# Kernel optimization log

Measured on AMD Instinct MI355X. Metric: run time of the kernel, lower is better.

Reference implementation:

```python
import jax, jax.numpy as jnp
import numpy as np
from jax import lax

NUM_CLASSES = 80
TOPK = 1000
CONF_THRESH = 0.05
NMS_THRESH = 0.6
MAX_COORD = 4096.0  # > any box coordinate; used for class-aware NMS offset trick
N_ANCHORS = 262144


def setup_inputs() -> dict:
    key = jax.random.key(0)
    k1, k2, k3 = jax.random.split(key, 3)
    # classification logits; shift down so sigmoid scores are mostly below conf_thresh
    cls_pred = jax.random.normal(k1, (1, N_ANCHORS, NUM_CLASSES), jnp.float32) * 2.0 - 2.0
    # valid xyxy boxes in absolute pixel coords (image ~1024)
    xy = jax.random.uniform(k2, (1, N_ANCHORS, 2), jnp.float32) * 1000.0
    wh = jax.random.uniform(k3, (1, N_ANCHORS, 2), jnp.float32) * 200.0 + 4.0
    box_pred = jnp.concatenate([xy, xy + wh], axis=-1)
    return {"cls_pred": cls_pred, "box_pred": box_pred, "img_h": 1024, "img_w": 1024}


def _pairwise_iou(b):
    # b: [K, 4] xyxy -> [K, K] IoU
    x1, y1, x2, y2 = b[:, 0], b[:, 1], b[:, 2], b[:, 3]
    area = (x2 - x1) * (y2 - y1)
    ix1 = jnp.maximum(x1[:, None], x1[None, :])
    iy1 = jnp.maximum(y1[:, None], y1[None, :])
    ix2 = jnp.minimum(x2[:, None], x2[None, :])
    iy2 = jnp.minimum(y2[:, None], y2[None, :])
    inter = jnp.clip(ix2 - ix1, 0.0) * jnp.clip(iy2 - iy1, 0.0)
    return inter / (area[:, None] + area[None, :] - inter + 1e-9)


def reference(cls_pred, box_pred, img_h, img_w):
    cls_p = cls_pred[0]          # [N, C]
    box_p = box_pred[0]          # [N, 4]
    # sigmoid + flatten + descending sort + slice(topk)  ==  top_k on flat scores
    scores_all = jax.nn.sigmoid(cls_p).reshape(-1)            # [N*C]
    top_scores, top_idxs = lax.top_k(scores_all, TOPK)        # sorted descending
    valid = top_scores > CONF_THRESH                          # keep mask (fixed size)
    labels = top_idxs % NUM_CLASSES
    anchor_idxs = top_idxs // NUM_CLASSES
    boxes = box_p[anchor_idxs]                                # [K, 4]

    # class-aware (per-class) greedy NMS via coordinate offset trick
    offset = labels.astype(boxes.dtype)[:, None] * MAX_COORD
    iou = _pairwise_iou(boxes + offset)                       # [K, K]
    idx = jnp.arange(TOPK)

    def body(i, keep):
        sup = keep[i] & (iou[i] > NMS_THRESH) & (idx > i)
        return keep & ~sup

    keep = lax.fori_loop(0, TOPK, body, valid)

    # normalize boxes to [0, 1] by image size and clip (as inference_single_image)
    scale = jnp.array([img_w, img_h, img_w, img_h], dtype=boxes.dtype)
    boxes_norm = jnp.clip(boxes / scale, 0.0, 1.0)

    scores_out = jnp.where(keep, top_scores, 0.0)
    return boxes_norm, scores_out, labels, keep
```

## Files before the change

### kernel.cpp

```cpp
#include <hip/hip_runtime.h>
#include <stdint.h>

#define NUM_CLASSES 80u
#define TOPK 1000
#define CONF_T 0.05f
#define NMS_T 0.6f
#define MAX_COORD 4096.0f
#define TARGET 1152u
#define CAP 49152u
#define SRVCAP 2048u
#define STATIC_F 4.0f
#define STATIC_KEY 0xC0800000u
#define NBINS 4096
#define BINSH 13
#define LCAP 512u
#define PBLK 1024u

typedef unsigned long long ull;
typedef ull ull2 __attribute__((ext_vector_type(2)));

__device__ __forceinline__ uint32_t fkey(float x) {
  uint32_t k = __float_as_uint(x);
  return (k & 0x80000000u) ? ~k : (k | 0x80000000u);
}

__device__ __forceinline__ uint32_t suffix_scan_256(uint32_t v, uint32_t* part,
                                                    int t) {
  int lane = t & 63, wid = t >> 6;
#pragma unroll
  for (int off = 1; off < 64; off <<= 1) {
    uint32_t x = __shfl_down(v, off);
    if (lane + off < 64) v += x;
  }
  if (lane == 0) part[wid] = v;
  __syncthreads();
  if (wid == 0 && lane < 4) {
    uint32_t pv = part[lane];
#pragma unroll
    for (int off = 1; off < 4; off <<= 1) {
      uint32_t x = __shfl_down(pv, off);
      if (lane + off < 4) pv += x;
    }
    part[lane] = pv;
  }
  __syncthreads();
  uint32_t after = (wid < 3) ? part[wid + 1] : 0u;
  return v + after;
}

template <int NBINSX>
__device__ __forceinline__ void pick_bin(const uint32_t* hl, uint32_t target,
                                         int t, uint32_t* part, uint32_t* binS,
                                         uint32_t* AS, uint32_t* cntS) {
  const int CH = NBINSX / 256;
  uint32_t s = 0;
#pragma unroll
  for (int j = 0; j < CH; ++j) s += hl[t * CH + j];
  uint32_t incl = suffix_scan_256(s, part, t);
  uint32_t after = incl - s;
  if (incl >= target && after < target) {
    uint32_t cum = after;
    for (int j = CH - 1; j >= 0; --j) {
      uint32_t h = hl[t * CH + j];
      if (cum + h >= target) { *binS = (uint32_t)(t * CH + j); *AS = cum; *cntS = h; break; }
      cum += h;
    }
  }
}

__global__ void __launch_bounds__(256) kz(uint32_t* sel, float* out,
                                          float* topScore) {
  int g = blockIdx.x * 256 + threadIdx.x;
  if (g < 16) sel[g] = 0u;
  for (int i = g; i < 4000; i += 4096) out[i] = 0.0f;
  if (g < 1000) { out[5000 + g] = 0.0f; topScore[g] = 0.0f; }
}

__global__ void __launch_bounds__(256) kA(const float4* __restrict__ cls, int n4,
                                          uint32_t* __restrict__ sel,
                                          uint32_t* __restrict__ candKey,
                                          uint32_t* __restrict__ candIdx) {
  __shared__ uint32_t lk[LCAP];
  __shared__ uint32_t li[LCAP];
  __shared__ uint32_t lcnt, gbase;
  if (threadIdx.x == 0) lcnt = 0u;
  __syncthreads();
  int stride = gridDim.x * blockDim.x;
  for (int i = blockIdx.x * blockDim.x + threadIdx.x; i < n4; i += stride) {
    float4 v = cls[i];
    float f4[4] = {v.x, v.y, v.z, v.w};
#pragma unroll
    for (int c = 0; c < 4; ++c) {
      if (f4[c] >= STATIC_F) {
        uint32_t p = atomicAdd(&lcnt, 1u);
        if (p < LCAP) { lk[p] = fkey(f4[c]); li[p] = (uint32_t)i * 4u + c; }
        else {
          uint32_t gp = atomicAdd(&sel[2], 1u);
          if (gp < CAP) { candKey[gp] = fkey(f4[c]); candIdx[gp] = (uint32_t)i * 4u + c; }
        }
      }
    }
  }
  __syncthreads();
  uint32_t c = lcnt; if (c > LCAP) c = LCAP;
  if (threadIdx.x == 0 && c) gbase = atomicAdd(&sel[2], c);
  __syncthreads();
  for (uint32_t i = threadIdx.x; i < c; i += 256u) {
    uint32_t gp = gbase + i;
    if (gp < CAP) { candKey[gp] = lk[i]; candIdx[gp] = li[i]; }
  }
}

__global__ void __launch_bounds__(256) kSel(
    const float4* __restrict__ cls4, int n4,
    uint32_t* __restrict__ sel,
    const uint32_t* __restrict__ candKey, const uint32_t* __restrict__ candIdx,
    ull* __restrict__ srv) {
  __shared__ uint32_t hl[NBINS];
  __shared__ uint32_t part[16];
  __shared__ uint32_t sk_[PBLK];
  __shared__ uint32_t si_[PBLK];
  __shared__ uint32_t lcnt, gbase, binS, AS, cntS;
  int t = threadIdx.x;
  uint32_t n = sel[2];
  bool fb = (n < TARGET) || (n > CAP);

  if (!fb) {
    for (int i = t; i < NBINS; i += 256) hl[i] = 0u;
    if (t == 0) { lcnt = 0u; binS = 0u; AS = 0u; cntS = 0u; }
    __syncthreads();
    const uint4* ck4 = (const uint4*)candKey;
    uint32_t n4c = n >> 2;
    for (uint32_t i = t; i < n4c; i += 256u) {
      uint4 kv = ck4[i];
      uint32_t b0 = (kv.x - STATIC_KEY) >> BINSH; if (b0 > NBINS - 1u) b0 = NBINS - 1u;
      uint32_t b1 = (kv.y - STATIC_KEY) >> BINSH; if (b1 > NBINS - 1u) b1 = NBINS - 1u;
      uint32_t b2 = (kv.z - STATIC_KEY) >> BINSH; if (b2 > NBINS - 1u) b2 = NBINS - 1u;
      uint32_t b3 = (kv.w - STATIC_KEY) >> BINSH; if (b3 > NBINS - 1u) b3 = NBINS - 1u;
      atomicAdd(&hl[b0], 1u); atomicAdd(&hl[b1], 1u);
      atomicAdd(&hl[b2], 1u); atomicAdd(&hl[b3], 1u);
    }
    for (uint32_t i = (n4c << 2) + (uint32_t)t; i < n; i += 256u) {
      uint32_t b = (candKey[i] - STATIC_KEY) >> BINSH;
      if (b > NBINS - 1u) b = NBINS - 1u;
      atomicAdd(&hl[b], 1u);
    }
    __syncthreads();
    pick_bin<NBINS>(hl, TARGET, t, part, &binS, &AS, &cntS);
    __syncthreads();
    uint32_t T;
    if (AS + cntS > SRVCAP)
      T = STATIC_KEY + ((binS + 1u) << BINSH);
    else
      T = STATIC_KEY + (binS << BINSH);
    uint32_t stride = gridDim.x * blockDim.x;
    for (uint32_t i = blockIdx.x * 256u + (uint32_t)t; i < n; i += stride) {
      uint32_t k = candKey[i];
      if (k >= T) {
        uint32_t p = atomicAdd(&lcnt, 1u);
        if (p < PBLK) { sk_[p] = k; si_[p] = candIdx[i]; }
      }
    }
    __syncthreads();
    uint32_t c = lcnt; if (c > PBLK) c = PBLK;
    if (t == 0 && c) gbase = atomicAdd(&sel[4], c);
    __syncthreads();
    for (uint32_t i = t; i < c; i += 256u) {
      uint32_t k = sk_[i];
      float x = __uint_as_float(k & 0x7fffffffu);
      float p = 1.0f / (1.0f + expf(-x));
      uint32_t pos = gbase + i;
      if (pos < SRVCAP)
        srv[pos] = ((ull)__float_as_uint(p) << 32) | (ull)(uint32_t)(~si_[i]);
    }
  } else {
    if (blockIdx.x != 0) return;
    for (int i = t; i < NBINS; i += 256) hl[i] = 0u;
    if (t == 0) { binS = 0u; AS = 0u; cntS = 0u; }
    __syncthreads();
    for (int i = t; i < n4; i += 256) {
      float4 v = cls4[i];
      atomicAdd(&hl[fkey(v.x) >> 20], 1u);
      atomicAdd(&hl[fkey(v.y) >> 20], 1u);
      atomicAdd(&hl[fkey(v.z) >> 20], 1u);
      atomicAdd(&hl[fkey(v.w) >> 20], 1u);
    }
    __syncthreads();
    pick_bin<NBINS>(hl, TARGET, t, part, &binS, &AS, &cntS);
    __syncthreads();
    uint32_t b20 = binS, A = AS;
    for (int i = t; i < 1024; i += 256) hl[i] = 0u;
    if (t == 0) { binS = 0u; }
    __syncthreads();
    for (int i = t; i < n4; i += 256) {
      float4 v = cls4[i];
      uint32_t k4[4] = {fkey(v.x), fkey(v.y), fkey(v.z), fkey(v.w)};
#pragma unroll
      for (int c2 = 0; c2 < 4; ++c2)
        if ((k4[c2] >> 20) == b20) atomicAdd(&hl[(k4[c2] >> 10) & 1023u], 1u);
    }
    __syncthreads();
    uint32_t rem = TARGET - A;
    pick_bin<1024>(hl, rem, t, part, &binS, &AS, &cntS);
    __syncthreads();
    uint32_t T = (b20 << 20) | (binS << 10);
    for (int i = t; i < n4; i += 256) {
      float4 v = cls4[i];
      uint32_t k4[4] = {fkey(v.x), fkey(v.y), fkey(v.z), fkey(v.w)};
#pragma unroll
      for (int c2 = 0; c2 < 4; ++c2) {
        uint32_t k = k4[c2];
        if (k >= T) {
          uint32_t pos = atomicAdd(&sel[4], 1u);
          if (pos < SRVCAP) {
            float x = (k & 0x80000000u) ? __uint_as_float(k & 0x7fffffffu)
                                        : __uint_as_float(~k);
            float p = 1.0f / (1.0f + expf(-x));
            uint32_t idx = (uint32_t)i * 4u + c2;
            srv[pos] = ((ull)__float_as_uint(p) << 32) | (ull)(uint32_t)(~idx);
          }
        }
      }
    }
  }
}

__global__ void __launch_bounds__(256) kF2(
    const float* __restrict__ box, const int* __restrict__ ph,
    const int* __restrict__ pw, const uint32_t* __restrict__ sel,
    const ull* __restrict__ srv, float* __restrict__ out,
    float* __restrict__ topScore, float* __restrict__ obox) {
  __shared__ __align__(16) ull sk[SRVCAP];
  int t = threadIdx.x;
  uint32_t scount = sel[4]; if (scount > SRVCAP) scount = SRVCAP;
  uint32_t pad = (scount + 1u) & ~1u;
  for (uint32_t i = t; i < pad; i += 256u) sk[i] = (i < scount) ? srv[i] : 0ull;
  __syncthreads();
  uint32_t i = blockIdx.x * 256u + (uint32_t)t;
  if (i >= scount) return;
  ull my = sk[i];
  uint32_t rank = 0;
#pragma unroll 4
  for (uint32_t j = 0; j < pad; j += 2u) {
    ull2 v = *reinterpret_cast<const ull2*>(&sk[j]);
    rank += (v.x > my) + (v.y > my);
  }
  if (rank >= TOPK) return;
  uint32_t idx = ~(uint32_t)my;
  float p = __uint_as_float((uint32_t)(my >> 32));
  uint32_t label = idx % NUM_CLASSES;
  uint32_t anchor = idx / NUM_CLASSES;
  float W = (float)pw[0], H = (float)ph[0];
  float b0 = box[anchor * 4u + 0u], b1 = box[anchor * 4u + 1u];
  float b2 = box[anchor * 4u + 2u], b3 = box[anchor * 4u + 3u];
  out[rank * 4 + 0] = fminf(fmaxf(b0 / W, 0.0f), 1.0f);
  out[rank * 4 + 1] = fminf(fmaxf(b1 / H, 0.0f), 1.0f);
  out[rank * 4 + 2] = fminf(fmaxf(b2 / W, 0.0f), 1.0f);
  out[rank * 4 + 3] = fminf(fmaxf(b3 / H, 0.0f), 1.0f);
  out[5000 + rank] = (float)label;
  topScore[rank] = p;
  float off = (float)label * MAX_COORD;
  obox[rank * 4 + 0] = b0 + off; obox[rank * 4 + 1] = b1 + off;
  obox[rank * 4 + 2] = b2 + off; obox[rank * 4 + 3] = b3 + off;
}

__global__ void kG(const float* __restrict__ obox, ull* __restrict__ masks,
                   uint32_t* __restrict__ rowsum) {
  __shared__ uint32_t rsS;
  int i = blockIdx.x;
  if (threadIdx.x == 0) rsS = 0u;
  __syncthreads();
  float x1i = obox[i * 4 + 0], y1i = obox[i * 4 + 1];
  float x2i = obox[i * 4 + 2], y2i = obox[i * 4 + 3];
  float ai = (x2i - x1i) * (y2i - y1i);
  for (int base = 0; base < 1024; base += 256) {
    int jj = base + (int)threadIdx.x;
    bool bit = false;
    if (jj < TOPK && jj > i) {
      float x1j = obox[jj * 4 + 0], y1j = obox[jj * 4 + 1];
      float x2j = obox[jj * 4 + 2], y2j = obox[jj * 4 + 3];
      float aj = (x2j - x1j) * (y2j - y1j);
      float ix1 = fmaxf(x1i, x1j), iy1 = fmaxf(y1i, y1j);
      float ix2 = fminf(x2i, x2j), iy2 = fminf(y2i, y2j);
      float iw = fmaxf(ix2 - ix1, 0.0f), ih = fmaxf(iy2 - iy1, 0.0f);
      float inter = iw * ih;
      float iou = inter / (ai + aj - inter + 1e-9f);
      bit = iou > NMS_T;
    }
    ull m = __ballot(bit);
    if ((threadIdx.x & 63u) == 0u) {
      masks[i * 16 + (jj >> 6)] = m;
      if (m) atomicOr(&rsS, 1u << (jj >> 6));
    }
  }
  __syncthreads();
  if (threadIdx.x == 0) rowsum[i] = rsS;
}

__global__ void __launch_bounds__(256) kH(const float* __restrict__ topScore,
                                          const ull* __restrict__ masks,
                                          const uint32_t* __restrict__ rowsum,
                                          float* __restrict__ out) {
  __shared__ ull lmask[TOPK * 16];
  __shared__ uint32_t rsL[TOPK];
  __shared__ ull keepsh[16];
  int t = threadIdx.x;
  for (int i = t; i < TOPK; i += 256) rsL[i] = rowsum[i];
  if (t < 16) keepsh[t] = 0ull;
  __syncthreads();
  for (int i = t; i < TOPK * 16; i += 256) {
    lmask[i] = ((rsL[i >> 4] >> (i & 15)) & 1u) ? masks[i] : 0ull;
  }
  for (int base = 0; base < 1024; base += 256) {
    int r = base + t;
    bool v = (r < TOPK) && (topScore[r] > CONF_T);
    ull b = __ballot(v);
    if ((t & 63) == 0) keepsh[(base >> 6) + (t >> 6)] = b;
  }
  __syncthreads();
  if (t < 64) {
    ull kw = (t < 16) ? keepsh[t] : 0ull;
    ull nzw = 0ull;
    if (t < 16) {
      for (int b = 0; b < 64; ++b) {
        int r = t * 64 + b;
        if (r < TOPK && rsL[r]) nzw |= 1ull << b;
      }
    }
    for (int w = 0; w < 16; ++w) {
      ull cur = __shfl(kw, w) & __shfl(nzw, w);
      while (cur) {
        int b = __ffsll((long long)cur) - 1;
        int i = w * 64 + b;
        if (t < 16) kw &= ~lmask[i * 16 + t];
        ull nk = __shfl(kw, w);
        cur = nk & __shfl(nzw, w);
        cur &= (b == 63) ? 0ull : (~0ull << (b + 1));
      }
    }
    if (t < 16) keepsh[t] = kw;
  }
  __syncthreads();
  for (int r = t; r < TOPK; r += 256) {
    bool k = (keepsh[r >> 6] >> (r & 63)) & 1ull;
    float s = topScore[r];
    out[4000 + r] = k ? s : 0.0f;
    out[6000 + r] = k ? 1.0f : 0.0f;
  }
}

extern "C" void kernel_launch(void* const* d_in, const int* in_sizes, int n_in,
                              void* d_out, int out_size, void* d_ws, size_t ws_size,
                              hipStream_t stream) {
  const float* cls = (const float*)d_in[0];
  const float* box = (const float*)d_in[1];
  const int* ph = (const int*)d_in[2];
  const int* pw = (const int*)d_in[3];
  float* out = (float*)d_out;
  int n = in_sizes[0];

  uint8_t* w = (uint8_t*)d_ws;
  uint32_t* sel     = (uint32_t*)(w + 16384);
  uint32_t* candKey = (uint32_t*)(w + 20480);
  uint32_t* candIdx = (uint32_t*)(w + 20480 + (size_t)CAP * 4);
  ull*      srv     = (ull*)     (w + 20480 + (size_t)CAP * 8);
  float*    topScore= (float*)   (w + 20480 + (size_t)CAP * 8 + 16384);
  float*    obox    = (float*)   (w + 20480 + (size_t)CAP * 8 + 16384 + 4096);
  ull*      masks   = (ull*)     (w + 20480 + (size_t)CAP * 8 + 16384 + 4096 + 16384);
  uint32_t* rowsum  = (uint32_t*)(w + 20480 + (size_t)CAP * 8 + 16384 + 4096 + 16384 + 131072);

  kz  <<<16, 256, 0, stream>>>(sel, out, topScore);
  kA  <<<2048, 256, 0, stream>>>((const float4*)cls, n / 4, sel, candKey, candIdx);
  kSel<<<64, 256, 0, stream>>>((const float4*)cls, n / 4, sel, candKey, candIdx, srv);
  kF2 <<<SRVCAP / 256, 256, 0, stream>>>(box, ph, pw, sel, srv, out, topScore, obox);
  kG  <<<TOPK, 256, 0, stream>>>(obox, masks, rowsum);
  kH  <<<1, 256, 0, stream>>>(topScore, masks, rowsum, out);
}
```

Measured before the change: 192.5 us.

## Fuse threshold selection and rank-scatter into one kernel using shared memory

Merges the selection kernel and the rank/scatter kernel into a single kSF kernel. Each of 16 blocks redundantly rebuilds the histogram and collects the full survivor set into shared memory, then ranks only the survivors assigned to it by index modulo 16. Sigmoid is deferred to the final emit step. This removes one launch and the global srv round-trip, at the cost of redundant histogram and compaction work per block and fewer blocks for the O(n^2) rank step.

```diff
diff --git a/kernel.cpp b/kernel.cpp
--- a/kernel.cpp
+++ b/kernel.cpp
@@ -14,7 +14,7 @@
 #define NBINS 4096
 #define BINSH 13
 #define LCAP 512u
-#define PBLK 1024u
+#define SFBLK 16u
 
 typedef unsigned long long ull;
 typedef ull ull2 __attribute__((ext_vector_type(2)));
@@ -111,146 +111,19 @@
   }
 }
 
-__global__ void __launch_bounds__(256) kSel(
-    const float4* __restrict__ cls4, int n4,
-    uint32_t* __restrict__ sel,
-    const uint32_t* __restrict__ candKey, const uint32_t* __restrict__ candIdx,
-    ull* __restrict__ srv) {
-  __shared__ uint32_t hl[NBINS];
-  __shared__ uint32_t part[16];
-  __shared__ uint32_t sk_[PBLK];
-  __shared__ uint32_t si_[PBLK];
-  __shared__ uint32_t lcnt, gbase, binS, AS, cntS;
-  int t = threadIdx.x;
-  uint32_t n = sel[2];
-  bool fb = (n < TARGET) || (n > CAP);
-
-  if (!fb) {
-    for (int i = t; i < NBINS; i += 256) hl[i] = 0u;
-    if (t == 0) { lcnt = 0u; binS = 0u; AS = 0u; cntS = 0u; }
-    __syncthreads();
-    const uint4* ck4 = (const uint4*)candKey;
-    uint32_t n4c = n >> 2;
-    for (uint32_t i = t; i < n4c; i += 256u) {
-      uint4 kv = ck4[i];
-      uint32_t b0 = (kv.x - STATIC_KEY) >> BINSH; if (b0 > NBINS - 1u) b0 = NBINS - 1u;
-      uint32_t b1 = (kv.y - STATIC_KEY) >> BINSH; if (b1 > NBINS - 1u) b1 = NBINS - 1u;
-      uint32_t b2 = (kv.z - STATIC_KEY) >> BINSH; if (b2 > NBINS - 1u) b2 = NBINS - 1u;
-      uint32_t b3 = (kv.w - STATIC_KEY) >> BINSH; if (b3 > NBINS - 1u) b3 = NBINS - 1u;
-      atomicAdd(&hl[b0], 1u); atomicAdd(&hl[b1], 1u);
-      atomicAdd(&hl[b2], 1u); atomicAdd(&hl[b3], 1u);
-    }
-    for (uint32_t i = (n4c << 2) + (uint32_t)t; i < n; i += 256u) {
-      uint32_t b = (candKey[i] - STATIC_KEY) >> BINSH;
-      if (b > NBINS - 1u) b = NBINS - 1u;
-      atomicAdd(&hl[b], 1u);
-    }
-    __syncthreads();
-    pick_bin<NBINS>(hl, TARGET, t, part, &binS, &AS, &cntS);
-    __syncthreads();
-    uint32_t T;
-    if (AS + cntS > SRVCAP)
-      T = STATIC_KEY + ((binS + 1u) << BINSH);
-    else
-      T = STATIC_KEY + (binS << BINSH);
-    uint32_t stride = gridDim.x * blockDim.x;
-    for (uint32_t i = blockIdx.x * 256u + (uint32_t)t; i < n; i += stride) {
-      uint32_t k = candKey[i];
-      if (k >= T) {
-        uint32_t p = atomicAdd(&lcnt, 1u);
-        if (p < PBLK) { sk_[p] = k; si_[p] = candIdx[i]; }
-      }
-    }
-    __syncthreads();
-    uint32_t c = lcnt; if (c > PBLK) c = PBLK;
-    if (t == 0 && c) gbase = atomicAdd(&sel[4], c);
-    __syncthreads();
-    for (uint32_t i = t; i < c; i += 256u) {
-      uint32_t k = sk_[i];
-      float x = __uint_as_float(k & 0x7fffffffu);
-      float p = 1.0f / (1.0f + expf(-x));
-      uint32_t pos = gbase + i;
-      if (pos < SRVCAP)
-        srv[pos] = ((ull)__float_as_uint(p) << 32) | (ull)(uint32_t)(~si_[i]);
-    }
-  } else {
-    if (blockIdx.x != 0) return;
-    for (int i = t; i < NBINS; i += 256) hl[i] = 0u;
-    if (t == 0) { binS = 0u; AS = 0u; cntS = 0u; }
-    __syncthreads();
-    for (int i = t; i < n4; i += 256) {
-      float4 v = cls4[i];
-      atomicAdd(&hl[fkey(v.x) >> 20], 1u);
-      atomicAdd(&hl[fkey(v.y) >> 20], 1u);
-      atomicAdd(&hl[fkey(v.z) >> 20], 1u);
-      atomicAdd(&hl[fkey(v.w) >> 20], 1u);
-    }
-    __syncthreads();
-    pick_bin<NBINS>(hl, TARGET, t, part, &binS, &AS, &cntS);
-    __syncthreads();
-    uint32_t b20 = binS, A = AS;
-    for (int i = t; i < 1024; i += 256) hl[i] = 0u;
-    if (t == 0) { binS = 0u; }
-    __syncthreads();
-    for (int i = t; i < n4; i += 256) {
-      float4 v = cls4[i];
-      uint32_t k4[4] = {fkey(v.x), fkey(v.y), fkey(v.z), fkey(v.w)};
-#pragma unroll
-      for (int c2 = 0; c2 < 4; ++c2)
-        if ((k4[c2] >> 20) == b20) atomicAdd(&hl[(k4[c2] >> 10) & 1023u], 1u);
-    }
-    __syncthreads();
-    uint32_t rem = TARGET - A;
-    pick_bin<1024>(hl, rem, t, part, &binS, &AS, &cntS);
-    __syncthreads();
-    uint32_t T = (b20 << 20) | (binS << 10);
-    for (int i = t; i < n4; i += 256) {
-      float4 v = cls4[i];
-      uint32_t k4[4] = {fkey(v.x), fkey(v.y), fkey(v.z), fkey(v.w)};
-#pragma unroll
-      for (int c2 = 0; c2 < 4; ++c2) {
-        uint32_t k = k4[c2];
-        if (k >= T) {
-          uint32_t pos = atomicAdd(&sel[4], 1u);
-          if (pos < SRVCAP) {
-            float x = (k & 0x80000000u) ? __uint_as_float(k & 0x7fffffffu)
-                                        : __uint_as_float(~k);
-            float p = 1.0f / (1.0f + expf(-x));
-            uint32_t idx = (uint32_t)i * 4u + c2;
-            srv[pos] = ((ull)__float_as_uint(p) << 32) | (ull)(uint32_t)(~idx);
-          }
-        }
-      }
-    }
-  }
-}
-
-__global__ void __launch_bounds__(256) kF2(
-    const float* __restrict__ box, const int* __restrict__ ph,
-    const int* __restrict__ pw, const uint32_t* __restrict__ sel,
-    const ull* __restrict__ srv, float* __restrict__ out,
-    float* __restrict__ topScore, float* __restrict__ obox) {
-  __shared__ __align__(16) ull sk[SRVCAP];
-  int t = threadIdx.x;
-  uint32_t scount = sel[4]; if (scount > SRVCAP) scount = SRVCAP;
-  uint32_t pad = (scount + 1u) & ~1u;
-  for (uint32_t i = t; i < pad; i += 256u) sk[i] = (i < scount) ? srv[i] : 0ull;
-  __syncthreads();
-  uint32_t i = blockIdx.x * 256u + (uint32_t)t;
-  if (i >= scount) return;
-  ull my = sk[i];
-  uint32_t rank = 0;
-#pragma unroll 4
-  for (uint32_t j = 0; j < pad; j += 2u) {
-    ull2 v = *reinterpret_cast<const ull2*>(&sk[j]);
-    rank += (v.x > my) + (v.y > my);
-  }
-  if (rank >= TOPK) return;
+__device__ __forceinline__ void emit_one(ull my, uint32_t rank,
+                                         const float* __restrict__ box,
+                                         float W, float H,
+                                         float* __restrict__ out,
+                                         float* __restrict__ topScore,
+                                         float* __restrict__ obox) {
   uint32_t idx = ~(uint32_t)my;
-  float p = __uint_as_float((uint32_t)(my >> 32));
+  uint32_t kk = (uint32_t)(my >> 32);
+  float x = (kk & 0x80000000u) ? __uint_as_float(kk & 0x7fffffffu)
+                               : __uint_as_float(~kk);
+  float p = 1.0f / (1.0f + expf(-x));
   uint32_t label = idx % NUM_CLASSES;
   uint32_t anchor = idx / NUM_CLASSES;
-  float W = (float)pw[0], H = (float)ph[0];
   float b0 = box[anchor * 4u + 0u], b1 = box[anchor * 4u + 1u];
   float b2 = box[anchor * 4u + 2u], b3 = box[anchor * 4u + 3u];
   out[rank * 4 + 0] = fminf(fmaxf(b0 / W, 0.0f), 1.0f);
@@ -262,6 +135,139 @@
   float off = (float)label * MAX_COORD;
   obox[rank * 4 + 0] = b0 + off; obox[rank * 4 + 1] = b1 + off;
   obox[rank * 4 + 2] = b2 + off; obox[rank * 4 + 3] = b3 + off;
+}
+
+__global__ void __launch_bounds__(256) kSF(
+    const float4* __restrict__ cls4, int n4,
+    const uint32_t* __restrict__ sel,
+    const uint32_t* __restrict__ candKey, const uint32_t* __restrict__ candIdx,
+    const float* __restrict__ box, const int* __restrict__ ph,
+    const int* __restrict__ pw, float* __restrict__ out,
+    float* __restrict__ topScore, float* __restrict__ obox) {
+  __shared__ uint32_t hl[NBINS];
+  __shared__ __align__(16) ull sk64[SRVCAP];
+  __shared__ uint32_t part[16];
+  __shared__ uint32_t lcnt, binS, AS, cntS;
+  int t = threadIdx.x;
+  uint32_t b = blockIdx.x;
+  uint32_t n = sel[2];
+  bool fb = (n < TARGET) || (n > CAP);
+  float W = (float)pw[0], H = (float)ph[0];
+
+  if (!fb) {
+    for (int i = t; i < NBINS; i += 256) hl[i] = 0u;
+    if (t == 0) { lcnt = 0u; binS = 0u; AS = 0u; cntS = 0u; }
+    __syncthreads();
+    const uint4* ck4 = (const uint4*)candKey;
+    uint32_t n4c = n >> 2;
+    for (uint32_t i = t; i < n4c; i += 256u) {
+      uint4 kv = ck4[i];
+      uint32_t b0 = (kv.x - STATIC_KEY) >> BINSH; if (b0 > NBINS - 1u) b0 = NBINS - 1u;
+      uint32_t b1 = (kv.y - STATIC_KEY) >> BINSH; if (b1 > NBINS - 1u) b1 = NBINS - 1u;
+      uint32_t b2 = (kv.z - STATIC_KEY) >> BINSH; if (b2 > NBINS - 1u) b2 = NBINS - 1u;
+      uint32_t b3 = (kv.w - STATIC_KEY) >> BINSH; if (b3 > NBINS - 1u) b3 = NBINS - 1u;
+      atomicAdd(&hl[b0], 1u); atomicAdd(&hl[b1], 1u);
+      atomicAdd(&hl[b2], 1u); atomicAdd(&hl[b3], 1u);
+    }
+    for (uint32_t i = (n4c << 2) + (uint32_t)t; i < n; i += 256u) {
+      uint32_t bb = (candKey[i] - STATIC_KEY) >> BINSH;
+      if (bb > NBINS - 1u) bb = NBINS - 1u;
+      atomicAdd(&hl[bb], 1u);
+    }
+    __syncthreads();
+    pick_bin<NBINS>(hl, TARGET, t, part, &binS, &AS, &cntS);
+    __syncthreads();
+    uint32_t T;
+    if (AS + cntS > SRVCAP)
+      T = STATIC_KEY + ((binS + 1u) << BINSH);
+    else
+      T = STATIC_KEY + (binS << BINSH);
+    for (uint32_t i = t; i < n; i += 256u) {
+      uint32_t k = candKey[i];
+      if (k >= T) {
+        uint32_t p = atomicAdd(&lcnt, 1u);
+        if (p < SRVCAP)
+          sk64[p] = ((ull)k << 32) | (ull)(uint32_t)(~candIdx[i]);
+      }
+    }
+    __syncthreads();
+    uint32_t c = lcnt; if (c > SRVCAP) c = SRVCAP;
+    if ((c & 1u) && t == 0) sk64[c] = 0ull;
+    __syncthreads();
+    uint32_t pad = (c + 1u) & ~1u;
+    for (uint32_t p = t; p < c; p += 256u) {
+      ull my = sk64[p];
+      uint32_t idx = ~(uint32_t)my;
+      if (idx % SFBLK != b) continue;
+      uint32_t rank = 0;
+#pragma unroll 4
+      for (uint32_t j = 0; j < pad; j += 2u) {
+        ull2 v = *reinterpret_cast<const ull2*>(&sk64[j]);
+        rank += (v.x > my) + (v.y > my);
+      }
+      if (rank < TOPK) emit_one(my, rank, box, W, H, out, topScore, obox);
+    }
+  } else {
+    if (b != 0) return;
+    for (int i = t; i < NBINS; i += 256) hl[i] = 0u;
+    if (t == 0) { lcnt = 0u; binS = 0u; AS = 0u; cntS = 0u; }
+    __syncthreads();
+    for (int i = t; i < n4; i += 256) {
+      float4 v = cls4[i];
+      atomicAdd(&hl[fkey(v.x) >> 20], 1u);
+      atomicAdd(&hl[fkey(v.y) >> 20], 1u);
+      atomicAdd(&hl[fkey(v.z) >> 20], 1u);
+      atomicAdd(&hl[fkey(v.w) >> 20], 1u);
+    }
+    __syncthreads();
+    pick_bin<NBINS>(hl, TARGET, t, part, &binS, &AS, &cntS);
+    __syncthreads();
+    uint32_t b20 = binS, A = AS;
+    for (int i = t; i < 1024; i += 256) hl[i] = 0u;
+    if (t == 0) { binS = 0u; }
+    __syncthreads();
+    for (int i = t; i < n4; i += 256) {
+      float4 v = cls4[i];
+      uint32_t k4[4] = {fkey(v.x), fkey(v.y), fkey(v.z), fkey(v.w)};
+#pragma unroll
+      for (int c2 = 0; c2 < 4; ++c2)
+        if ((k4[c2] >> 20) == b20) atomicAdd(&hl[(k4[c2] >> 10) & 1023u], 1u);
+    }
+    __syncthreads();
+    uint32_t rem = TARGET - A;
+    pick_bin<1024>(hl, rem, t, part, &binS, &AS, &cntS);
+    __syncthreads();
+    uint32_t T = (b20 << 20) | (binS << 10);
+    for (int i = t; i < n4; i += 256) {
+      float4 v = cls4[i];
+      uint32_t k4[4] = {fkey(v.x), fkey(v.y), fkey(v.z), fkey(v.w)};
+#pragma unroll
+      for (int c2 = 0; c2 < 4; ++c2) {
+        uint32_t k = k4[c2];
+        if (k >= T) {
+          uint32_t p = atomicAdd(&lcnt, 1u);
+          if (p < SRVCAP) {
+            uint32_t idx = (uint32_t)i * 4u + c2;
+            sk64[p] = ((ull)k << 32) | (ull)(uint32_t)(~idx);
+          }
+        }
+      }
+    }
+    __syncthreads();
+    uint32_t c = lcnt; if (c > SRVCAP) c = SRVCAP;
+    if ((c & 1u) && t == 0) sk64[c] = 0ull;
+    __syncthreads();
+    uint32_t pad = (c + 1u) & ~1u;
+    for (uint32_t p = t; p < c; p += 256u) {
+      ull my = sk64[p];
+      uint32_t rank = 0;
+      for (uint32_t j = 0; j < pad; j += 2u) {
+        ull2 v = *reinterpret_cast<const ull2*>(&sk64[j]);
+        rank += (v.x > my) + (v.y > my);
+      }
+      if (rank < TOPK) emit_one(my, rank, box, W, H, out, topScore, obox);
+    }
+  }
 }
 
 __global__ void kG(const float* __restrict__ obox, ull* __restrict__ masks,
@@ -363,16 +369,15 @@
   uint32_t* sel     = (uint32_t*)(w + 16384);
   uint32_t* candKey = (uint32_t*)(w + 20480);
   uint32_t* candIdx = (uint32_t*)(w + 20480 + (size_t)CAP * 4);
-  ull*      srv     = (ull*)     (w + 20480 + (size_t)CAP * 8);
-  float*    topScore= (float*)   (w + 20480 + (size_t)CAP * 8 + 16384);
-  float*    obox    = (float*)   (w + 20480 + (size_t)CAP * 8 + 16384 + 4096);
-  ull*      masks   = (ull*)     (w + 20480 + (size_t)CAP * 8 + 16384 + 4096 + 16384);
-  uint32_t* rowsum  = (uint32_t*)(w + 20480 + (size_t)CAP * 8 + 16384 + 4096 + 16384 + 131072);
+  float*    topScore= (float*)   (w + 20480 + (size_t)CAP * 8);
+  float*    obox    = (float*)   (w + 20480 + (size_t)CAP * 8 + 4096);
+  ull*      masks   = (ull*)     (w + 20480 + (size_t)CAP * 8 + 4096 + 16384);
+  uint32_t* rowsum  = (uint32_t*)(w + 20480 + (size_t)CAP * 8 + 4096 + 16384 + 131072);
 
   kz  <<<16, 256, 0, stream>>>(sel, out, topScore);
   kA  <<<2048, 256, 0, stream>>>((const float4*)cls, n / 4, sel, candKey, candIdx);
-  kSel<<<64, 256, 0, stream>>>((const float4*)cls, n / 4, sel, candKey, candIdx, srv);
-  kF2 <<<SRVCAP / 256, 256, 0, stream>>>(box, ph, pw, sel, srv, out, topScore, obox);
+  kSF <<<SFBLK, 256, 0, stream>>>((const float4*)cls, n / 4, sel, candKey, candIdx,
+                                  box, ph, pw, out, topScore, obox);
   kG  <<<TOPK, 256, 0, stream>>>(obox, masks, rowsum);
   kH  <<<1, 256, 0, stream>>>(topScore, masks, rowsum, out);
 }
```

New measurement: 340.6 us. 1.77x slower.

## Replace global atomic candidate compaction with fixed per-block slots and fold zero-init

Applied to the files above, without the earlier changes.

kA now writes each block's candidates into a fixed slot region (48 per block) with a per-block count, instead of appending through a global atomic counter. kSel uses 1024-thread blocks, derives the total from the counts, scans the fixed slot array, and falls back to the full-histogram path if any block overflows its slots. The separate zeroing kernel is removed: counters are cleared in kA and the output/topScore zeroing moves into kSel. kH is widened to 1024 threads. The cost is scanning a padded slot array, plus a correctness risk if zeroing sel in kA block 0 races with other blocks, or if the output zeroing no longer covers every path.

```diff
diff --git a/kernel.cpp b/kernel.cpp
--- a/kernel.cpp
+++ b/kernel.cpp
@@ -7,14 +7,16 @@
 #define NMS_T 0.6f
 #define MAX_COORD 4096.0f
 #define TARGET 1152u
-#define CAP 49152u
+#define NBLK_A 2048u
+#define SLOTS 48u
+#define LINCAP (NBLK_A * SLOTS)
 #define SRVCAP 2048u
 #define STATIC_F 4.0f
 #define STATIC_KEY 0xC0800000u
 #define NBINS 4096
 #define BINSH 13
-#define LCAP 512u
-#define PBLK 1024u
+#define LCAP 64u
+#define PBLK 1536u
 
 typedef unsigned long long ull;
 typedef ull ull2 __attribute__((ext_vector_type(2)));
@@ -24,8 +26,8 @@
   return (k & 0x80000000u) ? ~k : (k | 0x80000000u);
 }
 
-__device__ __forceinline__ uint32_t suffix_scan_256(uint32_t v, uint32_t* part,
-                                                    int t) {
+__device__ __forceinline__ uint32_t suffix_scan_1024(uint32_t v, uint32_t* part,
+                                                     int t) {
   int lane = t & 63, wid = t >> 6;
 #pragma unroll
   for (int off = 1; off < 64; off <<= 1) {
@@ -34,56 +36,53 @@
   }
   if (lane == 0) part[wid] = v;
   __syncthreads();
-  if (wid == 0 && lane < 4) {
-    uint32_t pv = part[lane];
-#pragma unroll
-    for (int off = 1; off < 4; off <<= 1) {
+  if (wid == 0) {
+    uint32_t pv = (lane < 16) ? part[lane] : 0u;
+#pragma unroll
+    for (int off = 1; off < 16; off <<= 1) {
       uint32_t x = __shfl_down(pv, off);
-      if (lane + off < 4) pv += x;
-    }
-    part[lane] = pv;
-  }
-  __syncthreads();
-  uint32_t after = (wid < 3) ? part[wid + 1] : 0u;
+      if (lane + off < 16) pv += x;
+    }
+    if (lane < 16) part[lane] = pv;
+  }
+  __syncthreads();
+  uint32_t after = (wid < 15) ? part[wid + 1] : 0u;
   return v + after;
 }
 
 template <int NBINSX>
-__device__ __forceinline__ void pick_bin(const uint32_t* hl, uint32_t target,
-                                         int t, uint32_t* part, uint32_t* binS,
-                                         uint32_t* AS, uint32_t* cntS) {
-  const int CH = NBINSX / 256;
+__device__ __forceinline__ void pick_bin1024(const uint32_t* hl, uint32_t target,
+                                             int t, uint32_t* part,
+                                             uint32_t* binS, uint32_t* AS,
+                                             uint32_t* cntS) {
+  const int CH = NBINSX / 1024;
+  uint32_t cc[CH];
   uint32_t s = 0;
 #pragma unroll
-  for (int j = 0; j < CH; ++j) s += hl[t * CH + j];
-  uint32_t incl = suffix_scan_256(s, part, t);
+  for (int j = 0; j < CH; ++j) { cc[j] = hl[t * CH + j]; s += cc[j]; }
+  uint32_t incl = suffix_scan_1024(s, part, t);
   uint32_t after = incl - s;
   if (incl >= target && after < target) {
     uint32_t cum = after;
     for (int j = CH - 1; j >= 0; --j) {
-      uint32_t h = hl[t * CH + j];
-      if (cum + h >= target) { *binS = (uint32_t)(t * CH + j); *AS = cum; *cntS = h; break; }
-      cum += h;
-    }
-  }
-}
-
-__global__ void __launch_bounds__(256) kz(uint32_t* sel, float* out,
-                                          float* topScore) {
-  int g = blockIdx.x * 256 + threadIdx.x;
-  if (g < 16) sel[g] = 0u;
-  for (int i = g; i < 4000; i += 4096) out[i] = 0.0f;
-  if (g < 1000) { out[5000 + g] = 0.0f; topScore[g] = 0.0f; }
+      if (cum + cc[j] >= target) {
+        *binS = (uint32_t)(t * CH + j); *AS = cum; *cntS = cc[j]; break;
+      }
+      cum += cc[j];
+    }
+  }
 }
 
 __global__ void __launch_bounds__(256) kA(const float4* __restrict__ cls, int n4,
                                           uint32_t* __restrict__ sel,
+                                          uint32_t* __restrict__ cnt,
                                           uint32_t* __restrict__ candKey,
                                           uint32_t* __restrict__ candIdx) {
   __shared__ uint32_t lk[LCAP];
   __shared__ uint32_t li[LCAP];
-  __shared__ uint32_t lcnt, gbase;
+  __shared__ uint32_t lcnt;
   if (threadIdx.x == 0) lcnt = 0u;
+  if (blockIdx.x == 0 && threadIdx.x < 16) sel[threadIdx.x] = 0u;
   __syncthreads();
   int stride = gridDim.x * blockDim.x;
   for (int i = blockIdx.x * blockDim.x + threadIdx.x; i < n4; i += stride) {
@@ -94,78 +93,81 @@
       if (f4[c] >= STATIC_F) {
         uint32_t p = atomicAdd(&lcnt, 1u);
         if (p < LCAP) { lk[p] = fkey(f4[c]); li[p] = (uint32_t)i * 4u + c; }
-        else {
-          uint32_t gp = atomicAdd(&sel[2], 1u);
-          if (gp < CAP) { candKey[gp] = fkey(f4[c]); candIdx[gp] = (uint32_t)i * 4u + c; }
-        }
-      }
-    }
-  }
-  __syncthreads();
-  uint32_t c = lcnt; if (c > LCAP) c = LCAP;
-  if (threadIdx.x == 0 && c) gbase = atomicAdd(&sel[2], c);
-  __syncthreads();
-  for (uint32_t i = threadIdx.x; i < c; i += 256u) {
-    uint32_t gp = gbase + i;
-    if (gp < CAP) { candKey[gp] = lk[i]; candIdx[gp] = li[i]; }
-  }
-}
-
-__global__ void __launch_bounds__(256) kSel(
+      }
+    }
+  }
+  __syncthreads();
+  uint32_t c = lcnt;
+  if (threadIdx.x == 0) cnt[blockIdx.x] = c;
+  uint32_t m = c; if (m > SLOTS) m = SLOTS;
+  uint32_t base = blockIdx.x * SLOTS;
+  for (uint32_t i = threadIdx.x; i < SLOTS; i += 256u)
+    candKey[base + i] = (i < m) ? lk[i] : 0u;
+  for (uint32_t i = threadIdx.x; i < m; i += 256u)
+    candIdx[base + i] = li[i];
+}
+
+__global__ void __launch_bounds__(1024) kSel(
     const float4* __restrict__ cls4, int n4,
-    uint32_t* __restrict__ sel,
+    uint32_t* __restrict__ sel, const uint32_t* __restrict__ cnt,
     const uint32_t* __restrict__ candKey, const uint32_t* __restrict__ candIdx,
-    ull* __restrict__ srv) {
+    ull* __restrict__ srv, float* __restrict__ out,
+    float* __restrict__ topScore) {
   __shared__ uint32_t hl[NBINS];
   __shared__ uint32_t part[16];
   __shared__ uint32_t sk_[PBLK];
   __shared__ uint32_t si_[PBLK];
-  __shared__ uint32_t lcnt, gbase, binS, AS, cntS;
+  __shared__ uint32_t lcnt, gbase, binS, AS, cntS, ovS;
   int t = threadIdx.x;
-  uint32_t n = sel[2];
-  bool fb = (n < TARGET) || (n > CAP);
+  uint32_t b = blockIdx.x;
+
+  uint32_t c0 = cnt[t], c1 = cnt[t + 1024];
+  if (t == 0) { lcnt = 0u; binS = 0u; AS = 0u; cntS = 0u; ovS = 0u; }
+  for (int i = t; i < NBINS; i += 1024) hl[i] = 0u;
+  __syncthreads();
+  if (c0 > SLOTS || c1 > SLOTS) atomicOr(&ovS, 1u);
+  uint32_t m0 = c0 > SLOTS ? SLOTS : c0, m1 = c1 > SLOTS ? SLOTS : c1;
+  (void)suffix_scan_1024(m0 + m1, part, t);
+  uint32_t total = part[0];
+  bool fb = (ovS != 0u) || (total < TARGET);
 
   if (!fb) {
-    for (int i = t; i < NBINS; i += 256) hl[i] = 0u;
-    if (t == 0) { lcnt = 0u; binS = 0u; AS = 0u; cntS = 0u; }
-    __syncthreads();
     const uint4* ck4 = (const uint4*)candKey;
-    uint32_t n4c = n >> 2;
-    for (uint32_t i = t; i < n4c; i += 256u) {
+    for (uint32_t i = t; i < LINCAP / 4u; i += 1024u) {
       uint4 kv = ck4[i];
-      uint32_t b0 = (kv.x - STATIC_KEY) >> BINSH; if (b0 > NBINS - 1u) b0 = NBINS - 1u;
-      uint32_t b1 = (kv.y - STATIC_KEY) >> BINSH; if (b1 > NBINS - 1u) b1 = NBINS - 1u;
-      uint32_t b2 = (kv.z - STATIC_KEY) >> BINSH; if (b2 > NBINS - 1u) b2 = NBINS - 1u;
-      uint32_t b3 = (kv.w - STATIC_KEY) >> BINSH; if (b3 > NBINS - 1u) b3 = NBINS - 1u;
-      atomicAdd(&hl[b0], 1u); atomicAdd(&hl[b1], 1u);
-      atomicAdd(&hl[b2], 1u); atomicAdd(&hl[b3], 1u);
-    }
-    for (uint32_t i = (n4c << 2) + (uint32_t)t; i < n; i += 256u) {
-      uint32_t b = (candKey[i] - STATIC_KEY) >> BINSH;
-      if (b > NBINS - 1u) b = NBINS - 1u;
-      atomicAdd(&hl[b], 1u);
-    }
-    __syncthreads();
-    pick_bin<NBINS>(hl, TARGET, t, part, &binS, &AS, &cntS);
-    __syncthreads();
-    uint32_t T;
-    if (AS + cntS > SRVCAP)
-      T = STATIC_KEY + ((binS + 1u) << BINSH);
-    else
-      T = STATIC_KEY + (binS << BINSH);
-    uint32_t stride = gridDim.x * blockDim.x;
-    for (uint32_t i = blockIdx.x * 256u + (uint32_t)t; i < n; i += stride) {
+      uint32_t kk[4] = {kv.x, kv.y, kv.z, kv.w};
+#pragma unroll
+      for (int q = 0; q < 4; ++q) {
+        uint32_t k = kk[q];
+        if (k >= STATIC_KEY) {
+          uint32_t bb = (k - STATIC_KEY) >> BINSH;
+          if (bb > NBINS - 1u) bb = NBINS - 1u;
+          atomicAdd(&hl[bb], 1u);
+        }
+      }
+    }
+    __syncthreads();
+    pick_bin1024<NBINS>(hl, TARGET, t, part, &binS, &AS, &cntS);
+    __syncthreads();
+    bool bump = (AS + cntS > SRVCAP);
+    uint32_t T = STATIC_KEY + ((binS + (bump ? 1u : 0u)) << BINSH);
+    if (bump && b == 0) {
+      for (int i = t; i < 4000; i += 1024) out[i] = 0.0f;
+      for (int i = t; i < 1000; i += 1024) { out[5000 + i] = 0.0f; topScore[i] = 0.0f; }
+    }
+    uint32_t lo = b * (LINCAP / 64u), hi = lo + (LINCAP / 64u);
+    for (uint32_t i = lo + t; i < hi; i += 1024u) {
       uint32_t k = candKey[i];
       if (k >= T) {
         uint32_t p = atomicAdd(&lcnt, 1u);
-        if (p < PBLK) { sk_[p] = k; si_[p] = candIdx[i]; }
-      }
-    }
-    __syncthreads();
-    uint32_t c = lcnt; if (c > PBLK) c = PBLK;
+        sk_[p] = k; si_[p] = candIdx[i];
+      }
+    }
+    __syncthreads();
+    uint32_t c = lcnt;
     if (t == 0 && c) gbase = atomicAdd(&sel[4], c);
     __syncthreads();
-    for (uint32_t i = t; i < c; i += 256u) {
+    for (uint32_t i = t; i < c; i += 1024u) {
       uint32_t k = sk_[i];
       float x = __uint_as_float(k & 0x7fffffffu);
       float p = 1.0f / (1.0f + expf(-x));
@@ -174,11 +176,11 @@
         srv[pos] = ((ull)__float_as_uint(p) << 32) | (ull)(uint32_t)(~si_[i]);
     }
   } else {
-    if (blockIdx.x != 0) return;
-    for (int i = t; i < NBINS; i += 256) hl[i] = 0u;
+    if (b != 0) return;
+    for (int i = t; i < NBINS; i += 1024) hl[i] = 0u;
     if (t == 0) { binS = 0u; AS = 0u; cntS = 0u; }
     __syncthreads();
-    for (int i = t; i < n4; i += 256) {
+    for (int i = t; i < n4; i += 1024) {
       float4 v = cls4[i];
       atomicAdd(&hl[fkey(v.x) >> 20], 1u);
       atomicAdd(&hl[fkey(v.y) >> 20], 1u);
@@ -186,13 +188,13 @@
       atomicAdd(&hl[fkey(v.w) >> 20], 1u);
     }
     __syncthreads();
-    pick_bin<NBINS>(hl, TARGET, t, part, &binS, &AS, &cntS);
+    pick_bin1024<NBINS>(hl, TARGET, t, part, &binS, &AS, &cntS);
     __syncthreads();
     uint32_t b20 = binS, A = AS;
-    for (int i = t; i < 1024; i += 256) hl[i] = 0u;
-    if (t == 0) { binS = 0u; }
-    __syncthreads();
-    for (int i = t; i < n4; i += 256) {
+    hl[t] = 0u;
+    if (t == 0) binS = 0u;
+    __syncthreads();
+    for (int i = t; i < n4; i += 1024) {
       float4 v = cls4[i];
       uint32_t k4[4] = {fkey(v.x), fkey(v.y), fkey(v.z), fkey(v.w)};
 #pragma unroll
@@ -201,10 +203,12 @@
     }
     __syncthreads();
     uint32_t rem = TARGET - A;
-    pick_bin<1024>(hl, rem, t, part, &binS, &AS, &cntS);
+    pick_bin1024<1024>(hl, rem, t, part, &binS, &AS, &cntS);
     __syncthreads();
     uint32_t T = (b20 << 20) | (binS << 10);
-    for (int i = t; i < n4; i += 256) {
+    for (int i = t; i < 4000; i += 1024) out[i] = 0.0f;
+    for (int i = t; i < 1000; i += 1024) { out[5000 + i] = 0.0f; topScore[i] = 0.0f; }
+    for (int i = t; i < n4; i += 1024) {
       float4 v = cls4[i];
       uint32_t k4[4] = {fkey(v.x), fkey(v.y), fkey(v.z), fkey(v.w)};
 #pragma unroll
@@ -297,25 +301,23 @@
   if (threadIdx.x == 0) rowsum[i] = rsS;
 }
 
-__global__ void __launch_bounds__(256) kH(const float* __restrict__ topScore,
-                                          const ull* __restrict__ masks,
-                                          const uint32_t* __restrict__ rowsum,
-                                          float* __restrict__ out) {
+__global__ void __launch_bounds__(1024) kH(const float* __restrict__ topScore,
+                                           const ull* __restrict__ masks,
+                                           const uint32_t* __restrict__ rowsum,
+                                           float* __restrict__ out) {
   __shared__ ull lmask[TOPK * 16];
   __shared__ uint32_t rsL[TOPK];
   __shared__ ull keepsh[16];
   int t = threadIdx.x;
-  for (int i = t; i < TOPK; i += 256) rsL[i] = rowsum[i];
+  if (t < TOPK) rsL[t] = rowsum[t];
   if (t < 16) keepsh[t] = 0ull;
   __syncthreads();
-  for (int i = t; i < TOPK * 16; i += 256) {
+  for (int i = t; i < TOPK * 16; i += 1024)
     lmask[i] = ((rsL[i >> 4] >> (i & 15)) & 1u) ? masks[i] : 0ull;
-  }
-  for (int base = 0; base < 1024; base += 256) {
-    int r = base + t;
-    bool v = (r < TOPK) && (topScore[r] > CONF_T);
-    ull b = __ballot(v);
-    if ((t & 63) == 0) keepsh[(base >> 6) + (t >> 6)] = b;
+  {
+    bool v = (t < TOPK) && (topScore[t] > CONF_T);
+    ull bb = __ballot(v);
+    if ((t & 63) == 0) keepsh[t >> 6] = bb;
   }
   __syncthreads();
   if (t < 64) {
@@ -341,11 +343,11 @@
     if (t < 16) keepsh[t] = kw;
   }
   __syncthreads();
-  for (int r = t; r < TOPK; r += 256) {
-    bool k = (keepsh[r >> 6] >> (r & 63)) & 1ull;
-    float s = topScore[r];
-    out[4000 + r] = k ? s : 0.0f;
-    out[6000 + r] = k ? 1.0f : 0.0f;
+  if (t < TOPK) {
+    bool k = (keepsh[t >> 6] >> (t & 63)) & 1ull;
+    float s = topScore[t];
+    out[4000 + t] = k ? s : 0.0f;
+    out[6000 + t] = k ? 1.0f : 0.0f;
   }
 }
 
@@ -360,19 +362,19 @@
   int n = in_sizes[0];
 
   uint8_t* w = (uint8_t*)d_ws;
-  uint32_t* sel     = (uint32_t*)(w + 16384);
-  uint32_t* candKey = (uint32_t*)(w + 20480);
-  uint32_t* candIdx = (uint32_t*)(w + 20480 + (size_t)CAP * 4);
-  ull*      srv     = (ull*)     (w + 20480 + (size_t)CAP * 8);
-  float*    topScore= (float*)   (w + 20480 + (size_t)CAP * 8 + 16384);
-  float*    obox    = (float*)   (w + 20480 + (size_t)CAP * 8 + 16384 + 4096);
-  ull*      masks   = (ull*)     (w + 20480 + (size_t)CAP * 8 + 16384 + 4096 + 16384);
-  uint32_t* rowsum  = (uint32_t*)(w + 20480 + (size_t)CAP * 8 + 16384 + 4096 + 16384 + 131072);
-
-  kz  <<<16, 256, 0, stream>>>(sel, out, topScore);
-  kA  <<<2048, 256, 0, stream>>>((const float4*)cls, n / 4, sel, candKey, candIdx);
-  kSel<<<64, 256, 0, stream>>>((const float4*)cls, n / 4, sel, candKey, candIdx, srv);
+  uint32_t* cnt     = (uint32_t*)(w);
+  uint32_t* sel     = (uint32_t*)(w + 8192);
+  uint32_t* candKey = (uint32_t*)(w + 12288);
+  uint32_t* candIdx = (uint32_t*)(w + 12288 + (size_t)LINCAP * 4);
+  ull*      srv     = (ull*)     (w + 12288 + (size_t)LINCAP * 8);
+  float*    topScore= (float*)   (w + 12288 + (size_t)LINCAP * 8 + 16384);
+  float*    obox    = (float*)   (w + 12288 + (size_t)LINCAP * 8 + 16384 + 4096);
+  ull*      masks   = (ull*)     (w + 12288 + (size_t)LINCAP * 8 + 16384 + 4096 + 16384);
+  uint32_t* rowsum  = (uint32_t*)(w + 12288 + (size_t)LINCAP * 8 + 16384 + 4096 + 16384 + 131072);
+
+  kA  <<<NBLK_A, 256, 0, stream>>>((const float4*)cls, n / 4, sel, cnt, candKey, candIdx);
+  kSel<<<64, 1024, 0, stream>>>((const float4*)cls, n / 4, sel, cnt, candKey, candIdx, srv, out, topScore);
   kF2 <<<SRVCAP / 256, 256, 0, stream>>>(box, ph, pw, sel, srv, out, topScore, obox);
   kG  <<<TOPK, 256, 0, stream>>>(obox, masks, rowsum);
-  kH  <<<1, 256, 0, stream>>>(topScore, masks, rowsum, out);
-}
+  kH  <<<1, 1024, 0, stream>>>(topScore, masks, rowsum, out);
+}
```

Result: faster. 169.1 us (median of 2 runs) (-12.2%).
